# Optimization experiments

Hardware: AMD Instinct MI355X
Metric: run time of the kernel (lower is better)

## Reference

```python
import jax, jax.numpy as jnp
import numpy as np

DIM = 1024
DIM_HEAD = 128
HEADS = 8
DIM_INNER = DIM_HEAD * HEADS


def setup_inputs() -> dict:
    key = jax.random.key(0)
    k_x, k_qkv, k_out = jax.random.split(key, 3)
    x = jax.random.normal(k_x, (2, 2048, DIM), dtype=jnp.float32)
    gamma = jnp.ones((DIM,), dtype=jnp.float32)
    # nn.Linear weights stored as [out, in]; init ~ U(-1/sqrt(in), 1/sqrt(in))
    w_qkv = jax.random.uniform(k_qkv, (DIM_INNER * 3, DIM), dtype=jnp.float32,
                               minval=-1.0, maxval=1.0) / np.sqrt(DIM)
    w_out = jax.random.uniform(k_out, (DIM, DIM_INNER), dtype=jnp.float32,
                               minval=-1.0, maxval=1.0) / np.sqrt(DIM_INNER)
    return {"x": x, "gamma": gamma, "w_qkv": w_qkv, "w_out": w_out}


def reference(x, gamma, w_qkv, w_out):
    scale_norm = DIM ** 0.5
    scale_attn = DIM_HEAD ** -0.5
    # RMSNorm as written: F.normalize (L2) * sqrt(dim) * gamma
    l2 = jnp.sqrt(jnp.sum(x * x, axis=-1, keepdims=True))
    xn = x / jnp.maximum(l2, 1e-12) * scale_norm * gamma
    # QKV projection: [b, n, 3*h*d]
    qkv = jnp.einsum('bnc,fc->bnf', xn, w_qkv)
    b, n, _ = qkv.shape
    qkv = qkv.reshape(b, n, 3, HEADS, DIM_HEAD)
    q, k, v = (qkv[:, :, 0], qkv[:, :, 1], qkv[:, :, 2])  # [b, n, h, d]
    q = q * scale_attn
    sim = jnp.einsum('bihd,bjhd->bhij', q, k)
    causal_mask = jnp.triu(jnp.ones((n, n), dtype=bool), k=1)
    neg = -jnp.finfo(sim.dtype).max
    sim = jnp.where(causal_mask, neg, sim)
    attn = jax.nn.softmax(sim, axis=-1)
    out = jnp.einsum('bhij,bjhd->bihd', attn, v)
    out = out.reshape(b, n, DIM_INNER)  # merge heads: b n (h d)
    return jnp.einsum('bnf,cf->bnc', out, w_out)
```

## Files before the change

### kernel.cpp

```cpp
#include <hip/hip_runtime.h>

#define SEQ 2048
#define NTOK 4096
#define DIM 1024
#define FQKV 3072
#define SC_ATTN 0.08838834764831843f
#define SC_Q (0.08838834764831843f * 1.4426950408889634f)
#define SC_NORM 32.0f

typedef short short8 __attribute__((ext_vector_type(8)));
typedef float f32x4 __attribute__((ext_vector_type(4)));
typedef unsigned short u16x4 __attribute__((ext_vector_type(4)));

__device__ __forceinline__ unsigned short f2bf(float f) {
    unsigned int u = __float_as_uint(f);
    u += 0x7fffu + ((u >> 16) & 1u);
    return (unsigned short)(u >> 16);
}
__device__ __forceinline__ float bf2f(unsigned short b) {
    return __uint_as_float(((unsigned int)b) << 16);
}
__device__ __forceinline__ void gl_lds16(const void* g, void* l) {
    __builtin_amdgcn_global_load_lds((const __attribute__((address_space(1))) void*)g,
                                     (__attribute__((address_space(3))) void*)l, 16, 0, 0);
}

__global__ __launch_bounds__(256) void l2norm_bf16(const float* __restrict__ x,
                                                   const float* __restrict__ gamma,
                                                   unsigned short* __restrict__ xn) {
    int token = blockIdx.x;
    float4 v = ((const float4*)(x + (size_t)token * DIM))[threadIdx.x];
    float ss = v.x * v.x + v.y * v.y + v.z * v.z + v.w * v.w;
#pragma unroll
    for (int off = 32; off > 0; off >>= 1) ss += __shfl_down(ss, off);
    __shared__ float wsum[4];
    if ((threadIdx.x & 63) == 0) wsum[threadIdx.x >> 6] = ss;
    __syncthreads();
    float tot = wsum[0] + wsum[1] + wsum[2] + wsum[3];
    float sc = SC_NORM / fmaxf(sqrtf(tot), 1e-12f);
    float4 g = ((const float4*)gamma)[threadIdx.x];
    u16x4 o;
    o.x = f2bf(v.x * sc * g.x);
    o.y = f2bf(v.y * sc * g.y);
    o.z = f2bf(v.z * sc * g.z);
    o.w = f2bf(v.w * sc * g.w);
    ((u16x4*)(xn + (size_t)token * DIM))[threadIdx.x] = o;
}

__global__ __launch_bounds__(256) void wconv(const float* __restrict__ w,
                                             unsigned short* __restrict__ o, int n4) {
    int i = blockIdx.x * 256 + threadIdx.x;
    if (i >= n4) return;
    float4 v = ((const float4*)w)[i];
    u16x4 r;
    r.x = f2bf(v.x); r.y = f2bf(v.y); r.z = f2bf(v.z); r.w = f2bf(v.w);
    ((u16x4*)o)[i] = r;
}

template<int C_MODE>
__global__ __launch_bounds__(256) void gemm_bf16(const unsigned short* __restrict__ A,
                                                 const unsigned short* __restrict__ B,
                                                 void* __restrict__ Cv,
                                                 int M, int N, int K) {
    __shared__ unsigned short As[2][128 * 64];
    __shared__ unsigned short Bs[2][128 * 64];
    const int bn = blockIdx.x * 128, bm = blockIdx.y * 128;
    const int tid = threadIdx.x, lane = tid & 63, wv = tid >> 6;
    const int wr = wv >> 1, wc = wv & 1;
    const int l15 = lane & 15, g = lane >> 4;

    f32x4 acc[4][4] = {};

    auto stage = [&](int buf, int k0) {
#pragma unroll
        for (int inst = 0; inst < 4; ++inst) {
            int ci = inst * 256 + wv * 64 + lane;
            int row = ci >> 3, cc = ci & 7;
            int co = (cc ^ (row & 7)) << 3;
            gl_lds16(A + (size_t)(bm + row) * K + k0 + co, &As[buf][(inst * 256 + wv * 64) * 8]);
            gl_lds16(B + (size_t)(bn + row) * K + k0 + co, &Bs[buf][(inst * 256 + wv * 64) * 8]);
        }
    };

    stage(0, 0);
    __syncthreads();
    int cur = 0;
    for (int k0 = 0; k0 < K; k0 += 64) {
        if (k0 + 64 < K) stage(cur ^ 1, k0 + 64);
#pragma unroll
        for (int ks = 0; ks < 2; ++ks) {
            short8 af[4], bf[4];
#pragma unroll
            for (int f = 0; f < 4; ++f) {
                int ra = wr * 64 + f * 16 + l15;
                af[f] = *(const short8*)&As[cur][ra * 64 + (((ks * 4 + g) ^ (ra & 7)) << 3)];
                int rb = wc * 64 + f * 16 + l15;
                bf[f] = *(const short8*)&Bs[cur][rb * 64 + (((ks * 4 + g) ^ (rb & 7)) << 3)];
            }
#pragma unroll
            for (int i = 0; i < 4; ++i)
#pragma unroll
                for (int j = 0; j < 4; ++j)
                    acc[i][j] = __builtin_amdgcn_mfma_f32_16x16x32_bf16(af[i], bf[j], acc[i][j], 0, 0, 0);
        }
        __syncthreads();
        cur ^= 1;
    }

    if (C_MODE == 0) {
        float* C = (float*)Cv;
#pragma unroll
        for (int i = 0; i < 4; ++i)
#pragma unroll
            for (int j = 0; j < 4; ++j)
#pragma unroll
                for (int v = 0; v < 4; ++v) {
                    int row = bm + wr * 64 + i * 16 + g * 4 + v;
                    int col = bn + wc * 64 + j * 16 + l15;
                    C[(size_t)row * N + col] = acc[i][j][v];
                }
    } else {
        unsigned short* C = (unsigned short*)Cv;
        float s = (bn < 1024) ? SC_Q : 1.0f;
#pragma unroll
        for (int i = 0; i < 4; ++i)
#pragma unroll
            for (int j = 0; j < 4; ++j)
#pragma unroll
                for (int v = 0; v < 4; ++v) {
                    int row = bm + wr * 64 + i * 16 + g * 4 + v;
                    int col = bn + wc * 64 + j * 16 + l15;
                    C[(size_t)row * N + col] = f2bf(acc[i][j][v] * s);
                }
    }
}

__global__ __launch_bounds__(256) void transpose_v(const unsigned short* __restrict__ qkv,
                                                   unsigned short* __restrict__ vt) {
    __shared__ unsigned short T[64][72];
    const int t0 = blockIdx.x * 64, d0 = blockIdx.y * 64, bh = blockIdx.z;
    const int b = bh >> 3, h = bh & 7;
    const int tid = threadIdx.x;
#pragma unroll
    for (int p = 0; p < 2; ++p) {
        int r = p * 32 + (tid >> 3), c = tid & 7;
        *(short8*)&T[r][c * 8] =
            *(const short8*)(qkv + (size_t)(b * SEQ + t0 + r) * FQKV + 2048 + h * 128 + d0 + c * 8);
    }
    __syncthreads();
#pragma unroll
    for (int p = 0; p < 2; ++p) {
        int d = p * 32 + (tid >> 3), c = tid & 7;
        short8 v;
#pragma unroll
        for (int j = 0; j < 8; ++j) v[j] = (short)T[c * 8 + j][d];
        *(short8*)(vt + (size_t)(bh * 128 + d0 + d) * SEQ + t0 + c * 8) = v;
    }
}

__global__ __launch_bounds__(256) void attn_mfma(const unsigned short* __restrict__ qkv,
                                                 const unsigned short* __restrict__ vt,
                                                 unsigned short* __restrict__ ao,
                                                 float* __restrict__ po,
                                                 float* __restrict__ pml) {
    __shared__ unsigned short Ks[64 * 128];
    __shared__ unsigned short Vs[128 * 64];
    __shared__ unsigned short Ps[4][16 * 64];
    const int h = blockIdx.y, b = blockIdx.z;
    const int x = blockIdx.x;
    int qblk, jb0, jb1, split, slot;
    if (x < 32) {
        qblk = 31 - (x >> 1);
        int s = x & 1;
        int T = qblk + 1, half = (T + 1) >> 1;
        jb0 = s ? half : 0;
        jb1 = s ? T : half;
        split = 1;
        slot = ((b * 8 + h) * 16 + (qblk - 16)) * 2 + s;
    } else {
        qblk = 47 - x;
        jb0 = 0; jb1 = qblk + 1;
        split = 0; slot = 0;
    }
    const int tid = threadIdx.x, lane = tid & 63, wv = tid >> 6;
    const int l15 = lane & 15, g = lane >> 4;
    const int q0 = qblk * 64;
    const int qrow = q0 + wv * 16 + l15;

    auto stage = [&](int jb) {
#pragma unroll
        for (int inst = 0; inst < 4; ++inst) {
            int ci = inst * 256 + wv * 64 + lane;
            int rowk = ci >> 4, ck = ci & 15;
            gl_lds16(qkv + (size_t)(b * SEQ + jb * 64 + rowk) * FQKV + 1024 + h * 128
                         + ((ck ^ (rowk & 7)) << 3),
                     &Ks[(inst * 256 + wv * 64) * 8]);
            int rowv = ci >> 3, cv = ci & 7;
            gl_lds16(vt + (size_t)((b * 8 + h) * 128 + rowv) * SEQ + jb * 64
                        + ((cv ^ (rowv & 7)) << 3),
                     &Vs[(inst * 256 + wv * 64) * 8]);
        }
    };

    short8 qf[4];
    {
        const unsigned short* qb = qkv + (size_t)(b * SEQ + qrow) * FQKV + h * 128;
#pragma unroll
        for (int ks = 0; ks < 4; ++ks) qf[ks] = *(const short8*)(qb + ks * 32 + g * 8);
    }

    float m_r = -1e30f, l_r = 0.f;
    f32x4 o[8] = {};

    for (int jb = jb0; jb < jb1; ++jb) {
        __syncthreads();
        stage(jb);
        __syncthreads();

        f32x4 s[4] = {};
        __builtin_amdgcn_s_setprio(1);
#pragma unroll
        for (int ks = 0; ks < 4; ++ks) {
#pragma unroll
            for (int fi = 0; fi < 4; ++fi) {
                int rk = fi * 16 + l15;
                short8 kf = *(const short8*)&Ks[rk * 128 + (((ks * 4 + g) ^ (rk & 7)) << 3)];
                s[fi] = __builtin_amdgcn_mfma_f32_16x16x32_bf16(kf, qf[ks], s[fi], 0, 0, 0);
            }
        }
        __builtin_amdgcn_s_setprio(0);

        if (jb == qblk) {
#pragma unroll
            for (int fi = 0; fi < 4; ++fi)
#pragma unroll
                for (int v = 0; v < 4; ++v) {
                    int kv = q0 + fi * 16 + g * 4 + v;
                    if (kv > qrow) s[fi][v] = -1e30f;
                }
        }

        float mx = -1e30f;
#pragma unroll
        for (int fi = 0; fi < 4; ++fi)
            mx = fmaxf(mx, fmaxf(fmaxf(s[fi][0], s[fi][1]), fmaxf(s[fi][2], s[fi][3])));
        mx = fmaxf(mx, __shfl_xor(mx, 16));
        mx = fmaxf(mx, __shfl_xor(mx, 32));
        float Mn = fmaxf(m_r, mx);
        float alpha = exp2f(m_r - Mn);
        m_r = Mn;

        float ps = 0.f;
#pragma unroll
        for (int fi = 0; fi < 4; ++fi) {
#pragma unroll
            for (int p2 = 0; p2 < 2; ++p2) {
                unsigned short b0 = f2bf(exp2f(s[fi][2 * p2] - Mn));
                unsigned short b1 = f2bf(exp2f(s[fi][2 * p2 + 1] - Mn));
                ps += bf2f(b0) + bf2f(b1);
                int kv = fi * 16 + g * 4 + 2 * p2;
                int addr = l15 * 64 + (((kv >> 3) ^ (l15 & 7)) << 3) + (kv & 7);
                *(unsigned int*)&Ps[wv][addr] = (unsigned int)b0 | ((unsigned int)b1 << 16);
            }
        }
        ps += __shfl_xor(ps, 16);
        ps += __shfl_xor(ps, 32);
        l_r = l_r * alpha + ps;

        float av[4];
#pragma unroll
        for (int v = 0; v < 4; ++v) av[v] = __shfl(alpha, g * 4 + v);
#pragma unroll
        for (int fn = 0; fn < 8; ++fn) {
            o[fn][0] *= av[0]; o[fn][1] *= av[1]; o[fn][2] *= av[2]; o[fn][3] *= av[3];
        }

        __builtin_amdgcn_s_setprio(1);
#pragma unroll
        for (int ks = 0; ks < 2; ++ks) {
            short8 pa = *(const short8*)&Ps[wv][l15 * 64 + (((ks * 4 + g) ^ (l15 & 7)) << 3)];
#pragma unroll
            for (int fn = 0; fn < 8; ++fn) {
                int rv = fn * 16 + l15;
                short8 vf = *(const short8*)&Vs[rv * 64 + (((ks * 4 + g) ^ (rv & 7)) << 3)];
                o[fn] = __builtin_amdgcn_mfma_f32_16x16x32_bf16(pa, vf, o[fn], 0, 0, 0);
            }
        }
        __builtin_amdgcn_s_setprio(0);
    }

    if (split) {
        float* od = po + (size_t)slot * (64 * 128);
#pragma unroll
        for (int fn = 0; fn < 8; ++fn)
#pragma unroll
            for (int v = 0; v < 4; ++v)
                od[(wv * 16 + g * 4 + v) * 128 + fn * 16 + l15] = o[fn][v];
        if (g == 0) {
            pml[(size_t)slot * 128 + wv * 16 + l15] = m_r;
            pml[(size_t)slot * 128 + 64 + wv * 16 + l15] = l_r;
        }
    } else {
        float lv[4];
#pragma unroll
        for (int v = 0; v < 4; ++v) lv[v] = 1.0f / __shfl(l_r, g * 4 + v);
#pragma unroll
        for (int fn = 0; fn < 8; ++fn)
#pragma unroll
            for (int v = 0; v < 4; ++v) {
                int row = b * SEQ + q0 + wv * 16 + g * 4 + v;
                ao[(size_t)row * DIM + h * 128 + fn * 16 + l15] = f2bf(o[fn][v] * lv[v]);
            }
    }
}

__global__ __launch_bounds__(256) void attn_combine(const float* __restrict__ po,
                                                    const float* __restrict__ pml,
                                                    unsigned short* __restrict__ ao) {
    int t = blockIdx.x;
    int qi = t & 15, h = (t >> 4) & 7, b = t >> 7;
    int qblk = 16 + qi;
    int slot0 = ((b * 8 + h) * 16 + qi) * 2;
    int row = threadIdx.x >> 2;
    int dp = threadIdx.x & 3;
    float m0 = pml[(size_t)slot0 * 128 + row];
    float l0 = pml[(size_t)slot0 * 128 + 64 + row];
    float m1 = pml[(size_t)(slot0 + 1) * 128 + row];
    float l1 = pml[(size_t)(slot0 + 1) * 128 + 64 + row];
    float M = fmaxf(m0, m1);
    float w0 = exp2f(m0 - M), w1 = exp2f(m1 - M);
    float inv = 1.0f / (w0 * l0 + w1 * l1);
    w0 *= inv; w1 *= inv;
    const float4* O0 = (const float4*)(po + (size_t)slot0 * 8192 + row * 128 + dp * 32);
    const float4* O1 = (const float4*)(po + (size_t)(slot0 + 1) * 8192 + row * 128 + dp * 32);
    unsigned short* dst = ao + ((size_t)(b * SEQ + qblk * 64 + row)) * DIM + h * 128 + dp * 32;
#pragma unroll
    for (int j = 0; j < 8; ++j) {
        float4 a = O0[j], c = O1[j];
        u16x4 r;
        r.x = f2bf(w0 * a.x + w1 * c.x);
        r.y = f2bf(w0 * a.y + w1 * c.y);
        r.z = f2bf(w0 * a.z + w1 * c.z);
        r.w = f2bf(w0 * a.w + w1 * c.w);
        *(u16x4*)(dst + j * 4) = r;
    }
}

extern "C" void kernel_launch(void* const* d_in, const int* in_sizes, int n_in,
                              void* d_out, int out_size, void* d_ws, size_t ws_size,
                              hipStream_t stream) {
    const float* x     = (const float*)d_in[0];
    const float* gamma = (const float*)d_in[1];
    const float* w_qkv = (const float*)d_in[2];
    const float* w_out = (const float*)d_in[3];

    char* ws = (char*)d_ws;
    unsigned short* qkvb = (unsigned short*)ws;
    unsigned short* vtb  = (unsigned short*)(ws + 25165824);
    unsigned short* xnb  = (unsigned short*)(ws + 33554432);
    unsigned short* wqb  = (unsigned short*)(ws + 41943040);
    unsigned short* wob  = (unsigned short*)(ws + 48234496);
    unsigned short* aob  = (unsigned short*)(ws + 50331648);
    float*          pml  = (float*)(ws + 58720256);
    float*          po   = (float*)d_out;

    wconv<<<3072, 256, 0, stream>>>(w_qkv, wqb, 786432);
    wconv<<<1024, 256, 0, stream>>>(w_out, wob, 262144);
    l2norm_bf16<<<4096, 256, 0, stream>>>(x, gamma, xnb);
    gemm_bf16<1><<<dim3(24, 32), 256, 0, stream>>>(xnb, wqb, qkvb, NTOK, FQKV, DIM);
    transpose_v<<<dim3(32, 2, 16), 256, 0, stream>>>(qkvb, vtb);
    attn_mfma<<<dim3(48, 8, 2), 256, 0, stream>>>(qkvb, vtb, aob, po, pml);
    attn_combine<<<256, 256, 0, stream>>>(po, pml, aob);
    gemm_bf16<0><<<dim3(8, 32), 256, 0, stream>>>(aob, wob, (float*)d_out, NTOK, DIM, DIM);
}
```

Measured before the change: 128.9 us.

## Prefetch next K/V tile into registers and skip unnecessary softmax rescaling

Replaces direct global-to-LDS staging with a register prefetch of the next K/V tile, issued before the current tile's compute and written to LDS after a barrier. This lets global load latency overlap with the MFMA and softmax work. The online softmax now rescales the running max and accumulators only when some row's max grows by more than 16 in log2 units, which removes most exp/multiply work per tile. Launch bounds now request 4 blocks per SM; combined with the extra prefetch registers this adds register pressure and may cause spills.

Result: slower. 183.1 us (+42.0%).

```diff
diff --git a/kernel.cpp b/kernel.cpp
--- a/kernel.cpp
+++ b/kernel.cpp
@@ -158,11 +158,11 @@
     }
 }
 
-__global__ __launch_bounds__(256) void attn_mfma(const unsigned short* __restrict__ qkv,
-                                                 const unsigned short* __restrict__ vt,
-                                                 unsigned short* __restrict__ ao,
-                                                 float* __restrict__ po,
-                                                 float* __restrict__ pml) {
+__global__ __launch_bounds__(256, 4) void attn_mfma(const unsigned short* __restrict__ qkv,
+                                                    const unsigned short* __restrict__ vt,
+                                                    unsigned short* __restrict__ ao,
+                                                    float* __restrict__ po,
+                                                    float* __restrict__ pml) {
     __shared__ unsigned short Ks[64 * 128];
     __shared__ unsigned short Vs[128 * 64];
     __shared__ unsigned short Ps[4][16 * 64];
@@ -187,18 +187,25 @@
     const int q0 = qblk * 64;
     const int qrow = q0 + wv * 16 + l15;
 
-    auto stage = [&](int jb) {
+    short8 kreg[4], vreg[4];
+    auto issue = [&](int jb) {
 #pragma unroll
         for (int inst = 0; inst < 4; ++inst) {
-            int ci = inst * 256 + wv * 64 + lane;
+            int ci = inst * 256 + tid;
             int rowk = ci >> 4, ck = ci & 15;
-            gl_lds16(qkv + (size_t)(b * SEQ + jb * 64 + rowk) * FQKV + 1024 + h * 128
-                         + ((ck ^ (rowk & 7)) << 3),
-                     &Ks[(inst * 256 + wv * 64) * 8]);
+            kreg[inst] = *(const short8*)(qkv + (size_t)(b * SEQ + jb * 64 + rowk) * FQKV
+                                          + 1024 + h * 128 + ((ck ^ (rowk & 7)) << 3));
             int rowv = ci >> 3, cv = ci & 7;
-            gl_lds16(vt + (size_t)((b * 8 + h) * 128 + rowv) * SEQ + jb * 64
-                        + ((cv ^ (rowv & 7)) << 3),
-                     &Vs[(inst * 256 + wv * 64) * 8]);
+            vreg[inst] = *(const short8*)(vt + (size_t)((b * 8 + h) * 128 + rowv) * SEQ
+                                          + jb * 64 + ((cv ^ (rowv & 7)) << 3));
+        }
+    };
+    auto commit = [&]() {
+#pragma unroll
+        for (int inst = 0; inst < 4; ++inst) {
+            int ci = inst * 256 + tid;
+            *(short8*)&Ks[ci * 8] = kreg[inst];
+            *(short8*)&Vs[ci * 8] = vreg[inst];
         }
     };
 
@@ -212,10 +219,12 @@
     float m_r = -1e30f, l_r = 0.f;
     f32x4 o[8] = {};
 
+    issue(jb0);
+    commit();
+    __syncthreads();
+
     for (int jb = jb0; jb < jb1; ++jb) {
-        __syncthreads();
-        stage(jb);
-        __syncthreads();
+        if (jb + 1 < jb1) issue(jb + 1);
 
         f32x4 s[4] = {};
         __builtin_amdgcn_s_setprio(1);
@@ -246,17 +255,27 @@
             mx = fmaxf(mx, fmaxf(fmaxf(s[fi][0], s[fi][1]), fmaxf(s[fi][2], s[fi][3])));
         mx = fmaxf(mx, __shfl_xor(mx, 16));
         mx = fmaxf(mx, __shfl_xor(mx, 32));
-        float Mn = fmaxf(m_r, mx);
-        float alpha = exp2f(m_r - Mn);
-        m_r = Mn;
+        if (__any(mx - m_r > 16.0f)) {
+            float Mn = fmaxf(m_r, mx);
+            float alpha = exp2f(m_r - Mn);
+            l_r *= alpha;
+            float av[4];
+#pragma unroll
+            for (int v = 0; v < 4; ++v) av[v] = __shfl(alpha, g * 4 + v);
+#pragma unroll
+            for (int fn = 0; fn < 8; ++fn) {
+                o[fn][0] *= av[0]; o[fn][1] *= av[1]; o[fn][2] *= av[2]; o[fn][3] *= av[3];
+            }
+            m_r = Mn;
+        }
 
         float ps = 0.f;
 #pragma unroll
         for (int fi = 0; fi < 4; ++fi) {
 #pragma unroll
             for (int p2 = 0; p2 < 2; ++p2) {
-                unsigned short b0 = f2bf(exp2f(s[fi][2 * p2] - Mn));
-                unsigned short b1 = f2bf(exp2f(s[fi][2 * p2 + 1] - Mn));
+                unsigned short b0 = f2bf(exp2f(s[fi][2 * p2] - m_r));
+                unsigned short b1 = f2bf(exp2f(s[fi][2 * p2 + 1] - m_r));
                 ps += bf2f(b0) + bf2f(b1);
                 int kv = fi * 16 + g * 4 + 2 * p2;
                 int addr = l15 * 64 + (((kv >> 3) ^ (l15 & 7)) << 3) + (kv & 7);
@@ -265,15 +284,7 @@
         }
         ps += __shfl_xor(ps, 16);
         ps += __shfl_xor(ps, 32);
-        l_r = l_r * alpha + ps;
-
-        float av[4];
-#pragma unroll
-        for (int v = 0; v < 4; ++v) av[v] = __shfl(alpha, g * 4 + v);
-#pragma unroll
-        for (int fn = 0; fn < 8; ++fn) {
-            o[fn][0] *= av[0]; o[fn][1] *= av[1]; o[fn][2] *= av[2]; o[fn][3] *= av[3];
-        }
+        l_r += ps;
 
         __builtin_amdgcn_s_setprio(1);
 #pragma unroll
@@ -287,6 +298,12 @@
             }
         }
         __builtin_amdgcn_s_setprio(0);
+
+        __syncthreads();
+        if (jb + 1 < jb1) {
+            commit();
+            __syncthreads();
+        }
     }
 
     if (split) {
```

## Overlap K/V staging in attention, add lazy softmax rescale, merge weight-conversion launches

Applied to the files above, without the earlier changes.

The attention loop now splits K and V staging. V for the current block is issued before QK^T, and K for the next block is loaded during the PV matmul, so global-to-LDS loads overlap with compute. The online softmax rescales the O accumulator and running sum only when any row's max grows by more than 16 (log2 units), which skips the per-iteration alpha multiply. The row sum now uses fp32 exponentials rather than bf16-rounded ones. The two weight-conversion kernels are merged into one launch. Risks: V is read from LDS after loads issued within the same iteration, with only a barrier and no explicit vmcnt wait, which could race. Also, the numerator P is rounded to bf16 while the denominator is summed in fp32.

Measured after the change: 123.5 us. 4.2% less time.

```diff
diff --git a/kernel.cpp b/kernel.cpp
--- a/kernel.cpp
+++ b/kernel.cpp
@@ -16,9 +16,6 @@
     unsigned int u = __float_as_uint(f);
     u += 0x7fffu + ((u >> 16) & 1u);
     return (unsigned short)(u >> 16);
-}
-__device__ __forceinline__ float bf2f(unsigned short b) {
-    return __uint_as_float(((unsigned int)b) << 16);
 }
 __device__ __forceinline__ void gl_lds16(const void* g, void* l) {
     __builtin_amdgcn_global_load_lds((const __attribute__((address_space(1))) void*)g,
@@ -47,14 +44,16 @@
     ((u16x4*)(xn + (size_t)token * DIM))[threadIdx.x] = o;
 }
 
-__global__ __launch_bounds__(256) void wconv(const float* __restrict__ w,
-                                             unsigned short* __restrict__ o, int n4) {
+__global__ __launch_bounds__(256) void wconv2(const float* __restrict__ wa, unsigned short* __restrict__ oa, int na4,
+                                              const float* __restrict__ wb, unsigned short* __restrict__ ob, int nb4) {
     int i = blockIdx.x * 256 + threadIdx.x;
-    if (i >= n4) return;
-    float4 v = ((const float4*)w)[i];
+    const float* w; unsigned short* o; int idx;
+    if (i < na4) { w = wa; o = oa; idx = i; }
+    else { idx = i - na4; if (idx >= nb4) return; w = wb; o = ob; }
+    float4 v = ((const float4*)w)[idx];
     u16x4 r;
     r.x = f2bf(v.x); r.y = f2bf(v.y); r.z = f2bf(v.z); r.w = f2bf(v.w);
-    ((u16x4*)o)[i] = r;
+    ((u16x4*)o)[idx] = r;
 }
 
 template<int C_MODE>
@@ -187,7 +186,7 @@
     const int q0 = qblk * 64;
     const int qrow = q0 + wv * 16 + l15;
 
-    auto stage = [&](int jb) {
+    auto stageK = [&](int jb) {
 #pragma unroll
         for (int inst = 0; inst < 4; ++inst) {
             int ci = inst * 256 + wv * 64 + lane;
@@ -195,6 +194,12 @@
             gl_lds16(qkv + (size_t)(b * SEQ + jb * 64 + rowk) * FQKV + 1024 + h * 128
                          + ((ck ^ (rowk & 7)) << 3),
                      &Ks[(inst * 256 + wv * 64) * 8]);
+        }
+    };
+    auto stageV = [&](int jb) {
+#pragma unroll
+        for (int inst = 0; inst < 4; ++inst) {
+            int ci = inst * 256 + wv * 64 + lane;
             int rowv = ci >> 3, cv = ci & 7;
             gl_lds16(vt + (size_t)((b * 8 + h) * 128 + rowv) * SEQ + jb * 64
                         + ((cv ^ (rowv & 7)) << 3),
@@ -212,10 +217,11 @@
     float m_r = -1e30f, l_r = 0.f;
     f32x4 o[8] = {};
 
+    stageK(jb0);
+    __syncthreads();
+
     for (int jb = jb0; jb < jb1; ++jb) {
-        __syncthreads();
-        stage(jb);
-        __syncthreads();
+        stageV(jb);
 
         f32x4 s[4] = {};
         __builtin_amdgcn_s_setprio(1);
@@ -246,18 +252,29 @@
             mx = fmaxf(mx, fmaxf(fmaxf(s[fi][0], s[fi][1]), fmaxf(s[fi][2], s[fi][3])));
         mx = fmaxf(mx, __shfl_xor(mx, 16));
         mx = fmaxf(mx, __shfl_xor(mx, 32));
-        float Mn = fmaxf(m_r, mx);
-        float alpha = exp2f(m_r - Mn);
-        m_r = Mn;
+        if (__any(mx - m_r > 16.0f)) {
+            float Mn = fmaxf(m_r, mx);
+            float alpha = exp2f(m_r - Mn);
+            l_r *= alpha;
+            float av[4];
+#pragma unroll
+            for (int v = 0; v < 4; ++v) av[v] = __shfl(alpha, g * 4 + v);
+#pragma unroll
+            for (int fn = 0; fn < 8; ++fn) {
+                o[fn][0] *= av[0]; o[fn][1] *= av[1]; o[fn][2] *= av[2]; o[fn][3] *= av[3];
+            }
+            m_r = Mn;
+        }
 
         float ps = 0.f;
 #pragma unroll
         for (int fi = 0; fi < 4; ++fi) {
 #pragma unroll
             for (int p2 = 0; p2 < 2; ++p2) {
-                unsigned short b0 = f2bf(exp2f(s[fi][2 * p2] - Mn));
-                unsigned short b1 = f2bf(exp2f(s[fi][2 * p2 + 1] - Mn));
-                ps += bf2f(b0) + bf2f(b1);
+                float e0 = exp2f(s[fi][2 * p2] - m_r);
+                float e1 = exp2f(s[fi][2 * p2 + 1] - m_r);
+                ps += e0 + e1;
+                unsigned short b0 = f2bf(e0), b1 = f2bf(e1);
                 int kv = fi * 16 + g * 4 + 2 * p2;
                 int addr = l15 * 64 + (((kv >> 3) ^ (l15 & 7)) << 3) + (kv & 7);
                 *(unsigned int*)&Ps[wv][addr] = (unsigned int)b0 | ((unsigned int)b1 << 16);
@@ -265,15 +282,10 @@
         }
         ps += __shfl_xor(ps, 16);
         ps += __shfl_xor(ps, 32);
-        l_r = l_r * alpha + ps;
-
-        float av[4];
-#pragma unroll
-        for (int v = 0; v < 4; ++v) av[v] = __shfl(alpha, g * 4 + v);
-#pragma unroll
-        for (int fn = 0; fn < 8; ++fn) {
-            o[fn][0] *= av[0]; o[fn][1] *= av[1]; o[fn][2] *= av[2]; o[fn][3] *= av[3];
-        }
+        l_r += ps;
+
+        __syncthreads();
+        if (jb + 1 < jb1) stageK(jb + 1);
 
         __builtin_amdgcn_s_setprio(1);
 #pragma unroll
@@ -287,6 +299,8 @@
             }
         }
         __builtin_amdgcn_s_setprio(0);
+
+        __syncthreads();
     }
 
     if (split) {
@@ -364,8 +378,7 @@
     float*          pml  = (float*)(ws + 58720256);
     float*          po   = (float*)d_out;
 
-    wconv<<<3072, 256, 0, stream>>>(w_qkv, wqb, 786432);
-    wconv<<<1024, 256, 0, stream>>>(w_out, wob, 262144);
+    wconv2<<<4096, 256, 0, stream>>>(w_qkv, wqb, 786432, w_out, wob, 262144);
     l2norm_bf16<<<4096, 256, 0, stream>>>(x, gamma, xnb);
     gemm_bf16<1><<<dim3(24, 32), 256, 0, stream>>>(xnb, wqb, qkvb, NTOK, FQKV, DIM);
     transpose_v<<<dim3(32, 2, 16), 256, 0, stream>>>(qkvb, vtb);
```
